# Kernel optimization log

Measured on AMD Instinct MI355X. Metric: run time of the kernel, lower is better.

Reference implementation:

```python
import jax, jax.numpy as jnp
import numpy as np

INPUT_DIM = 512
OUTPUT_DIM = 512
DEGREE = 8
BATCH = 16384


def setup_inputs() -> dict:
    key = jax.random.key(0)
    kx, kc = jax.random.split(key)
    x = jax.random.normal(kx, (BATCH, INPUT_DIM), dtype=jnp.float32)
    cheby_coeffs = jax.random.normal(kc, (INPUT_DIM, OUTPUT_DIM, DEGREE + 1), dtype=jnp.float32) / jnp.sqrt(
        jnp.float32(INPUT_DIM * (DEGREE + 1))
    )
    return {"x": x, "cheby_coeffs": cheby_coeffs}


def reference(x, cheby_coeffs):
    degree = cheby_coeffs.shape[-1] - 1
    arange = jnp.arange(degree + 1, dtype=x.dtype)  # [d]
    t = jnp.tanh(x)  # [b, i], squash into [-1, 1]
    theta = jnp.arccos(t)[..., None] * arange  # [b, i, d]
    basis = jnp.cos(theta)  # Chebyshev T_n(tanh(x)) = cos(n * arccos(tanh(x)))
    y = jnp.einsum('bid,iod->bo', basis, cheby_coeffs)
    return y
```

## Files before the change

### kernel.cpp

```cpp
#include <hip/hip_runtime.h>
#include <hip/hip_bf16.h>
#include <stdint.h>


#define BM 128
#define BN 128
#define NSTEPS 64
#define IN_DIM 512
#define OUT_DIM 512

typedef __attribute__((ext_vector_type(8))) short short8;
typedef __attribute__((ext_vector_type(4))) float f32x4;

__device__ __forceinline__ unsigned short f2bf(float f) {
  __hip_bfloat16 h = __float2bfloat16(f);
  return __builtin_bit_cast(unsigned short, h);
}

__device__ __forceinline__ float fast_tanh(float v) {
  float e = __expf(v + v);
  return 1.0f - 2.0f * __builtin_amdgcn_rcpf(e + 1.0f);
}

__device__ __forceinline__ void gload_lds16(const void* g, void* l) {
  __builtin_amdgcn_global_load_lds(
      (const __attribute__((address_space(1))) unsigned int*)(uintptr_t)g,
      (__attribute__((address_space(3))) unsigned int*)(uintptr_t)l,
      16, 0, 0);
}

__global__ __launch_bounds__(256) void cheby_reorder_b(
    const float* __restrict__ coeffs, unsigned char* __restrict__ bws) {
  const int g = blockIdx.x * 256 + threadIdx.x;
  const int i = g & 511;
  const int o = g >> 9;
  const int nb = o >> 7, nl = o & 127;
  const int itile = i >> 5, il = i & 31;
  const float* cp = coeffs + (size_t)i * 4608 + (size_t)o * 9;
  const int swz = (nl & 7) << 4;
#pragma unroll
  for (int p = 0; p < 4; ++p) {
    const size_t base =
        ((size_t)(nb * 64 + itile * 4 + p) << 14) + (size_t)nl * 128;
    *(unsigned short*)(bws + base + ((il * 2) ^ swz)) = f2bf(cp[1 + 2 * p]);
    *(unsigned short*)(bws + base + ((64 + il * 2) ^ swz)) =
        f2bf(cp[2 + 2 * p]);
  }
}

__global__ __launch_bounds__(64) void cheby_colsum(
    const float* __restrict__ coeffs, float* __restrict__ cs) {
  const int o = blockIdx.x;
  const int l = threadIdx.x;
  float s = 0.0f;
#pragma unroll
  for (int j = 0; j < 8; ++j)
    s += coeffs[(size_t)(l + j * 64) * 4608 + (size_t)o * 9];
#pragma unroll
  for (int off = 32; off > 0; off >>= 1) s += __shfl_down(s, off, 64);
  if (l == 0) cs[o] = s;
}

__global__ __launch_bounds__(256, 2) void cheby_gemm(
    const float* __restrict__ x, const unsigned char* __restrict__ bws,
    const float* __restrict__ colsum, float* __restrict__ out) {
  const int bid = blockIdx.x;
  const int m0 = (bid >> 2) * BM;
  const int nblk = bid & 3;
  const int n0 = nblk * BN;
  const int tid = threadIdx.x;
  const int lane = tid & 63;
  const int wid = tid >> 6;
  const int wm = (wid >> 1) * 64;
  const int wn = (wid & 1) * 64;
  const int l15 = lane & 15;
  const int lhi = lane >> 4;

  __shared__ __align__(16) unsigned char Bs[2][BN * 128];

  const float* xrow[4];
#pragma unroll
  for (int fm = 0; fm < 4; ++fm)
    xrow[fm] = x + (size_t)(m0 + wm + fm * 16 + l15) * IN_DIM + lhi * 8;

  float t2[4][8], Tm1[4][8], Tm2[4][8];
  f32x4 acc[4][4];
#pragma unroll
  for (int a = 0; a < 4; ++a)
#pragma unroll
    for (int b = 0; b < 4; ++b) acc[a][b] = (f32x4){0.f, 0.f, 0.f, 0.f};

  const unsigned char* bchunk0 = bws + ((size_t)(nblk * 64) << 14);
  const int goff = wid * 4096 + lane * 16;

  {
    const unsigned char* gsrc = bchunk0 + goff;
    unsigned char* ldst = &Bs[0][0] + wid * 4096;
    gload_lds16(gsrc, ldst);
    gload_lds16(gsrc + 1024, ldst + 1024);
    gload_lds16(gsrc + 2048, ldst + 2048);
    gload_lds16(gsrc + 3072, ldst + 3072);
  }

  for (int s = 0; s < NSTEPS; ++s) {
    const int p = s & 1;
    const int q = s & 3;

    float4 xa[4], xb[4];
    if (q == 0) {
      const int it = s >> 2;
#pragma unroll
      for (int fm = 0; fm < 4; ++fm) {
        const float* xp = xrow[fm] + it * 32;
        xa[fm] = reinterpret_cast<const float4*>(xp)[0];
        xb[fm] = reinterpret_cast<const float4*>(xp)[1];
      }
      __builtin_amdgcn_sched_barrier(0);
    }

    {
      const int snext = (s < NSTEPS - 1) ? s + 1 : NSTEPS - 1;
      const unsigned char* gsrc = bchunk0 + ((size_t)snext << 14) + goff;
      unsigned char* ldst = &Bs[p ^ 1][0] + wid * 4096;
      gload_lds16(gsrc, ldst);
      gload_lds16(gsrc + 1024, ldst + 1024);
      gload_lds16(gsrc + 2048, ldst + 2048);
      gload_lds16(gsrc + 3072, ldst + 3072);
    }

    if (q == 0) {
#pragma unroll
      for (int fm = 0; fm < 4; ++fm) {
#pragma unroll
        for (int j = 0; j < 8; ++j) {
          const float xv = (j < 4) ? ((const float*)&xa[fm])[j & 3]
                                   : ((const float*)&xb[fm])[j & 3];
          const float th = fast_tanh(xv);
          const float tt = th + th;
          t2[fm][j] = tt;
          Tm2[fm][j] = th;
          Tm1[fm][j] = __builtin_fmaf(tt, th, -1.0f);
        }
      }
    } else {
#pragma unroll
      for (int fm = 0; fm < 4; ++fm) {
#pragma unroll
        for (int j = 0; j < 8; ++j) {
          const float Ta = __builtin_fmaf(t2[fm][j], Tm1[fm][j], -Tm2[fm][j]);
          const float Tb = __builtin_fmaf(t2[fm][j], Ta, -Tm1[fm][j]);
          Tm2[fm][j] = Ta;
          Tm1[fm][j] = Tb;
        }
      }
    }
    short8 af0[4], af1[4];
#pragma unroll
    for (int fm = 0; fm < 4; ++fm)
#pragma unroll
      for (int j = 0; j < 8; ++j) {
        af0[fm][j] = (short)f2bf(Tm2[fm][j]);
        af1[fm][j] = (short)f2bf(Tm1[fm][j]);
      }

    asm volatile("s_waitcnt vmcnt(4)" ::: "memory");
    __builtin_amdgcn_s_barrier();

    const unsigned char* Bcur = &Bs[p][0];
#pragma unroll
    for (int fn = 0; fn < 4; ++fn) {
      const int row = wn + fn * 16 + l15;
      const int rsw = (row & 7) << 4;
      const short8 bf0 = *(const short8*)(
          Bcur + row * 128 + ((lhi * 16) ^ rsw));
      const short8 bf1 = *(const short8*)(
          Bcur + row * 128 + ((64 + lhi * 16) ^ rsw));
#pragma unroll
      for (int fm = 0; fm < 4; ++fm)
        acc[fm][fn] = __builtin_amdgcn_mfma_f32_16x16x32_bf16(
            af0[fm], bf0, acc[fm][fn], 0, 0, 0);
#pragma unroll
      for (int fm = 0; fm < 4; ++fm)
        acc[fm][fn] = __builtin_amdgcn_mfma_f32_16x16x32_bf16(
            af1[fm], bf1, acc[fm][fn], 0, 0, 0);
    }

    __builtin_amdgcn_s_barrier();
  }

  asm volatile("s_waitcnt vmcnt(0)" ::: "memory");

  float csv[4];
#pragma unroll
  for (int fn = 0; fn < 4; ++fn) csv[fn] = colsum[n0 + wn + fn * 16 + l15];
  const int lhi4 = lhi * 4;
#pragma unroll
  for (int fm = 0; fm < 4; ++fm) {
    const int r0 = m0 + wm + fm * 16 + lhi4;
#pragma unroll
    for (int fn = 0; fn < 4; ++fn) {
      const int col = n0 + wn + fn * 16 + l15;
#pragma unroll
      for (int r = 0; r < 4; ++r)
        out[(size_t)(r0 + r) * OUT_DIM + col] = acc[fm][fn][r] + csv[fn];
    }
  }
}

extern "C" void kernel_launch(void* const* d_in, const int* in_sizes, int n_in,
                              void* d_out, int out_size, void* d_ws,
                              size_t ws_size, hipStream_t stream) {
  const float* x = (const float*)d_in[0];
  const float* coeffs = (const float*)d_in[1];
  float* out = (float*)d_out;
  unsigned char* bws = (unsigned char*)d_ws;
  float* cs = (float*)((unsigned char*)d_ws + ((size_t)4 << 20));

  hipLaunchKernelGGL(cheby_reorder_b, dim3(1024), dim3(256), 0, stream, coeffs,
                     bws);
  hipLaunchKernelGGL(cheby_colsum, dim3(512), dim3(64), 0, stream, coeffs, cs);
  hipLaunchKernelGGL(cheby_gemm, dim3(512), dim3(256), 0, stream, x, bws, cs,
                     out);
}
```

Baseline: 113.2 us.

## Unroll K loop by four and compute next Chebyshev fragments after MFMA phase

Unrolls the 64-step main loop by four so the per-step branch on the tanh init and recurrence disappears. The A-fragment recurrence and bf16 packing for the next step now run right after the current MFMAs, overlapping VALU work with the matrix pipe. The x load for the next 32-column chunk is issued one sub-step early with an adjusted vmcnt wait. This changes register lifetimes, since packed fragments stay live across barriers, and could add register pressure under the 2-blocks-per-CU launch bound.

```diff
diff --git a/kernel.cpp b/kernel.cpp
--- a/kernel.cpp
+++ b/kernel.cpp
@@ -60,6 +60,74 @@
   for (int off = 32; off > 0; off >>= 1) s += __shfl_down(s, off, 64);
   if (l == 0) cs[o] = s;
 }
+
+#define ISSUE_B(SNEXT, PBUF)                                              \
+  {                                                                       \
+    const unsigned char* gsrc = bchunk0 + ((size_t)(SNEXT) << 14) + goff; \
+    unsigned char* ldst = &Bs[PBUF][0] + wid * 4096;                      \
+    gload_lds16(gsrc, ldst);                                              \
+    gload_lds16(gsrc + 1024, ldst + 1024);                                \
+    gload_lds16(gsrc + 2048, ldst + 2048);                                \
+    gload_lds16(gsrc + 3072, ldst + 3072);                                \
+  }
+
+#define MFMA_PHASE(PBUF)                                                   \
+  {                                                                        \
+    const unsigned char* Bcur = &Bs[PBUF][0];                              \
+    _Pragma("unroll") for (int fn = 0; fn < 4; ++fn) {                     \
+      const int row = wn + fn * 16 + l15;                                  \
+      const int rsw = (row & 7) << 4;                                      \
+      const short8 bf0 =                                                   \
+          *(const short8*)(Bcur + row * 128 + ((lhi * 16) ^ rsw));         \
+      const short8 bf1 =                                                   \
+          *(const short8*)(Bcur + row * 128 + ((64 + lhi * 16) ^ rsw));    \
+      _Pragma("unroll") for (int fm = 0; fm < 4; ++fm) acc[fm][fn] =       \
+          __builtin_amdgcn_mfma_f32_16x16x32_bf16(af0[fm], bf0,            \
+                                                  acc[fm][fn], 0, 0, 0);   \
+      _Pragma("unroll") for (int fm = 0; fm < 4; ++fm) acc[fm][fn] =       \
+          __builtin_amdgcn_mfma_f32_16x16x32_bf16(af1[fm], bf1,            \
+                                                  acc[fm][fn], 0, 0, 0);   \
+    }                                                                      \
+  }
+
+#define ADVANCE_PACK()                                                        \
+  {                                                                           \
+    _Pragma("unroll") for (int fm = 0; fm < 4; ++fm)                          \
+        _Pragma("unroll") for (int j = 0; j < 8; ++j) {                       \
+      const float Ta = __builtin_fmaf(t2[fm][j], Tm1[fm][j], -Tm2[fm][j]);    \
+      const float Tb = __builtin_fmaf(t2[fm][j], Ta, -Tm1[fm][j]);            \
+      Tm2[fm][j] = Ta;                                                        \
+      Tm1[fm][j] = Tb;                                                        \
+      af0[fm][j] = (short)f2bf(Ta);                                           \
+      af1[fm][j] = (short)f2bf(Tb);                                           \
+    }                                                                         \
+  }
+
+#define INIT_PACK()                                                           \
+  {                                                                           \
+    _Pragma("unroll") for (int fm = 0; fm < 4; ++fm)                          \
+        _Pragma("unroll") for (int j = 0; j < 8; ++j) {                       \
+      const float xv = (j < 4) ? ((const float*)&xa[fm])[j & 3]               \
+                               : ((const float*)&xb[fm])[j & 3];              \
+      const float th = fast_tanh(xv);                                         \
+      const float tt = th + th;                                               \
+      t2[fm][j] = tt;                                                         \
+      Tm2[fm][j] = th;                                                        \
+      Tm1[fm][j] = __builtin_fmaf(tt, th, -1.0f);                             \
+      af0[fm][j] = (short)f2bf(th);                                           \
+      af1[fm][j] = (short)f2bf(Tm1[fm][j]);                                   \
+    }                                                                         \
+  }
+
+#define LOAD_X(IT)                                                            \
+  {                                                                           \
+    _Pragma("unroll") for (int fm = 0; fm < 4; ++fm) {                        \
+      const float* xp = xrow[fm] + (IT) * 32;                                 \
+      xa[fm] = reinterpret_cast<const float4*>(xp)[0];                        \
+      xb[fm] = reinterpret_cast<const float4*>(xp)[1];                        \
+    }                                                                         \
+    __builtin_amdgcn_sched_barrier(0);                                        \
+  }
 
 __global__ __launch_bounds__(256, 2) void cheby_gemm(
     const float* __restrict__ x, const unsigned char* __restrict__ bws,
@@ -84,6 +152,8 @@
     xrow[fm] = x + (size_t)(m0 + wm + fm * 16 + l15) * IN_DIM + lhi * 8;
 
   float t2[4][8], Tm1[4][8], Tm2[4][8];
+  short8 af0[4], af1[4];
+  float4 xa[4], xb[4];
   f32x4 acc[4][4];
 #pragma unroll
   for (int a = 0; a < 4; ++a)
@@ -93,98 +163,36 @@
   const unsigned char* bchunk0 = bws + ((size_t)(nblk * 64) << 14);
   const int goff = wid * 4096 + lane * 16;
 
-  {
-    const unsigned char* gsrc = bchunk0 + goff;
-    unsigned char* ldst = &Bs[0][0] + wid * 4096;
-    gload_lds16(gsrc, ldst);
-    gload_lds16(gsrc + 1024, ldst + 1024);
-    gload_lds16(gsrc + 2048, ldst + 2048);
-    gload_lds16(gsrc + 3072, ldst + 3072);
-  }
-
-  for (int s = 0; s < NSTEPS; ++s) {
-    const int p = s & 1;
-    const int q = s & 3;
-
-    float4 xa[4], xb[4];
-    if (q == 0) {
-      const int it = s >> 2;
-#pragma unroll
-      for (int fm = 0; fm < 4; ++fm) {
-        const float* xp = xrow[fm] + it * 32;
-        xa[fm] = reinterpret_cast<const float4*>(xp)[0];
-        xb[fm] = reinterpret_cast<const float4*>(xp)[1];
-      }
-      __builtin_amdgcn_sched_barrier(0);
-    }
-
-    {
-      const int snext = (s < NSTEPS - 1) ? s + 1 : NSTEPS - 1;
-      const unsigned char* gsrc = bchunk0 + ((size_t)snext << 14) + goff;
-      unsigned char* ldst = &Bs[p ^ 1][0] + wid * 4096;
-      gload_lds16(gsrc, ldst);
-      gload_lds16(gsrc + 1024, ldst + 1024);
-      gload_lds16(gsrc + 2048, ldst + 2048);
-      gload_lds16(gsrc + 3072, ldst + 3072);
-    }
-
-    if (q == 0) {
-#pragma unroll
-      for (int fm = 0; fm < 4; ++fm) {
-#pragma unroll
-        for (int j = 0; j < 8; ++j) {
-          const float xv = (j < 4) ? ((const float*)&xa[fm])[j & 3]
-                                   : ((const float*)&xb[fm])[j & 3];
-          const float th = fast_tanh(xv);
-          const float tt = th + th;
-          t2[fm][j] = tt;
-          Tm2[fm][j] = th;
-          Tm1[fm][j] = __builtin_fmaf(tt, th, -1.0f);
-        }
-      }
-    } else {
-#pragma unroll
-      for (int fm = 0; fm < 4; ++fm) {
-#pragma unroll
-        for (int j = 0; j < 8; ++j) {
-          const float Ta = __builtin_fmaf(t2[fm][j], Tm1[fm][j], -Tm2[fm][j]);
-          const float Tb = __builtin_fmaf(t2[fm][j], Ta, -Tm1[fm][j]);
-          Tm2[fm][j] = Ta;
-          Tm1[fm][j] = Tb;
-        }
-      }
-    }
-    short8 af0[4], af1[4];
-#pragma unroll
-    for (int fm = 0; fm < 4; ++fm)
-#pragma unroll
-      for (int j = 0; j < 8; ++j) {
-        af0[fm][j] = (short)f2bf(Tm2[fm][j]);
-        af1[fm][j] = (short)f2bf(Tm1[fm][j]);
-      }
-
+  LOAD_X(0);
+  ISSUE_B(0, 0);
+  INIT_PACK();
+
+  for (int t = 0; t < 16; ++t) {
+    const int s0 = t * 4;
+    ISSUE_B(s0 + 1, 1);
     asm volatile("s_waitcnt vmcnt(4)" ::: "memory");
     __builtin_amdgcn_s_barrier();
-
-    const unsigned char* Bcur = &Bs[p][0];
-#pragma unroll
-    for (int fn = 0; fn < 4; ++fn) {
-      const int row = wn + fn * 16 + l15;
-      const int rsw = (row & 7) << 4;
-      const short8 bf0 = *(const short8*)(
-          Bcur + row * 128 + ((lhi * 16) ^ rsw));
-      const short8 bf1 = *(const short8*)(
-          Bcur + row * 128 + ((64 + lhi * 16) ^ rsw));
-#pragma unroll
-      for (int fm = 0; fm < 4; ++fm)
-        acc[fm][fn] = __builtin_amdgcn_mfma_f32_16x16x32_bf16(
-            af0[fm], bf0, acc[fm][fn], 0, 0, 0);
-#pragma unroll
-      for (int fm = 0; fm < 4; ++fm)
-        acc[fm][fn] = __builtin_amdgcn_mfma_f32_16x16x32_bf16(
-            af1[fm], bf1, acc[fm][fn], 0, 0, 0);
-    }
-
+    MFMA_PHASE(0);
+    ADVANCE_PACK();
+    __builtin_amdgcn_s_barrier();
+    ISSUE_B(s0 + 2, 0);
+    asm volatile("s_waitcnt vmcnt(4)" ::: "memory");
+    __builtin_amdgcn_s_barrier();
+    MFMA_PHASE(1);
+    ADVANCE_PACK();
+    __builtin_amdgcn_s_barrier();
+    LOAD_X((t < 15) ? t + 1 : 15);
+    ISSUE_B(s0 + 3, 1);
+    asm volatile("s_waitcnt vmcnt(12)" ::: "memory");
+    __builtin_amdgcn_s_barrier();
+    MFMA_PHASE(0);
+    ADVANCE_PACK();
+    __builtin_amdgcn_s_barrier();
+    ISSUE_B((t < 15) ? s0 + 4 : 63, 0);
+    asm volatile("s_waitcnt vmcnt(4)" ::: "memory");
+    __builtin_amdgcn_s_barrier();
+    MFMA_PHASE(1);
+    INIT_PACK();
     __builtin_amdgcn_s_barrier();
   }
 
```

Result: slower. 138.9 us (+22.7%).
